# Performance work log

Measured on AMD Instinct MI355X. Metric: run time of the kernel, lower is better.

Reference implementation:

```python
import jax, jax.numpy as jnp
import numpy as np

D_MODEL = 1024
NUM_HEADS = 16
HEAD_DIM = D_MODEL // NUM_HEADS
THETA = 10000.0
MAX_SEQ_LEN = 2048
BATCH = 4
SEQ = 2048


def _rope_tables():
    # theta_vec = 1 / theta**(arange(0, d_k, 2)/d_k), pos outer product
    inv_freq = 1.0 / (THETA ** (jnp.arange(0, HEAD_DIM, 2, dtype=jnp.float32) / HEAD_DIM))
    pos = jnp.arange(MAX_SEQ_LEN, dtype=jnp.float32)
    freqs = jnp.outer(pos, inv_freq)  # [max_seq, head_dim//2]
    return jnp.cos(freqs), jnp.sin(freqs)


def apply_rope(x, cos, sin):
    # x: [..., S, d]; cos/sin: [S, d//2]; interleaved pairwise rotation
    x1 = x[..., 0::2]
    x2 = x[..., 1::2]
    o1 = x1 * cos - x2 * sin
    o2 = x2 * cos + x1 * sin
    return jnp.stack([o1, o2], axis=-1).reshape(x.shape)


def setup_inputs() -> dict:
    key = jax.random.key(0)
    kx, kq, kk, kv, ko = jax.random.split(key, 5)
    std = (1.0 / D_MODEL) ** 0.5
    x = jax.random.normal(kx, (BATCH, SEQ, D_MODEL), dtype=jnp.float32)
    w_q = jax.random.normal(kq, (D_MODEL, D_MODEL), dtype=jnp.float32) * std
    w_k = jax.random.normal(kk, (D_MODEL, D_MODEL), dtype=jnp.float32) * std
    w_v = jax.random.normal(kv, (D_MODEL, D_MODEL), dtype=jnp.float32) * std
    w_o = jax.random.normal(ko, (D_MODEL, D_MODEL), dtype=jnp.float32) * std
    cos, sin = _rope_tables()
    return {"x": x, "w_q": w_q, "w_k": w_k, "w_v": w_v, "w_o": w_o,
            "cos": cos, "sin": sin}


def reference(x, w_q, w_k, w_v, w_o, cos, sin):
    b, s, d = x.shape
    h, dk = NUM_HEADS, HEAD_DIM

    def proj(w):
        # einsum '... s d, hd d -> ... s hd' == x @ w.T, then split heads
        y = jnp.einsum('bsd,ed->bse', x, w)
        return y.reshape(b, s, h, dk).transpose(0, 2, 1, 3)  # [b,h,s,dk]

    q = apply_rope(proj(w_q), cos[:s], sin[:s])
    k = apply_rope(proj(w_k), cos[:s], sin[:s])
    v = proj(w_v)

    scores = jnp.einsum('bhnd,bhmd->bhnm', q, k) / (dk ** 0.5)
    causal = jnp.tril(jnp.ones((s, s), dtype=bool))
    scores = jnp.where(causal, scores, -jnp.inf)
    attn = jax.nn.softmax(scores, axis=-1)
    out = jnp.einsum('bhnm,bhmd->bhnd', attn, v)  # [b,h,s,dk]
    out = out.transpose(0, 2, 1, 3).reshape(b, s, d)
    # einsum '... s hd, d hd -> ... s d' == out @ w_o.T
    return jnp.einsum('bse,de->bsd', out, w_o)
```

## Files before the change

### kernel.cpp

```cpp
#include <hip/hip_runtime.h>
#include <hip/hip_bf16.h>


typedef __bf16 bf16;
typedef __bf16 bf16x8 __attribute__((ext_vector_type(8)));
typedef __bf16 bf16x4 __attribute__((ext_vector_type(4)));
typedef float f32x4 __attribute__((ext_vector_type(4)));

#define LOG2E 1.4426950408889634f
#define QSCALE (0.125f * LOG2E * 8388608.0f)
#define SEXP_SEED ((126.94269504f - 16.0f * LOG2E) * 8388608.0f)

__device__ __forceinline__ void async16(const void* g, void* l) {
  __builtin_amdgcn_global_load_lds(
      (const __attribute__((address_space(1))) void*)g,
      (__attribute__((address_space(3))) void*)l, 16, 0, 0);
}

#define MFMA16(a, b, c) __builtin_amdgcn_mfma_f32_16x16x32_bf16(a, b, c, 0, 0, 0)

__global__ void cast_all_kernel(const float* __restrict__ x,
                                const float* __restrict__ wq,
                                const float* __restrict__ wk,
                                const float* __restrict__ wv,
                                const float* __restrict__ wo,
                                const float* __restrict__ cosT,
                                const float* __restrict__ sinT,
                                bf16* __restrict__ xb, bf16* __restrict__ wb,
                                float2* __restrict__ csT) {
  int i = blockIdx.x * blockDim.x + threadIdx.x;
  if (i >= 3145728) {
    int j = i - 3145728;
    float2 cs;
    cs.x = cosT[j];
    cs.y = sinT[j];
    csT[j] = cs;
    return;
  }
  const float* src;
  bf16* dst;
  long o;
  if (i < 2097152) {
    src = x; dst = xb; o = i;
  } else {
    long j = i - 2097152;
    int w = (int)(j >> 18);
    o = j & 262143;
    src = (w == 0) ? wq : (w == 1) ? wk : (w == 2) ? wv : wo;
    dst = wb + (long)w * 1048576;
  }
  float4 v = reinterpret_cast<const float4*>(src)[o];
  bf16x4 out;
  out.x = (bf16)v.x; out.y = (bf16)v.y; out.z = (bf16)v.z; out.w = (bf16)v.w;
  *reinterpret_cast<bf16x4*>(dst + o * 4) = out;
}

template <int EPI, int TM, int TN>
__device__ __forceinline__ void gemm_dev(const bf16* __restrict__ A,
                                         const bf16* __restrict__ B,
                                         void* __restrict__ C, int N, int K,
                                         int bm, int bn, bf16* As, bf16* Bs,
                                         const float2* __restrict__ csT) {
  constexpr int WM = TM / 64;
  constexpr int WN = 4 / WM;
  constexpr int CW = TN / WN;
  constexpr int NT = CW / 16;
  constexpr int ROUNDS = (TM + TN) / 64;
  const int tid = threadIdx.x;
  const int wid = tid >> 6, lane = tid & 63;
  const int quad = lane >> 4, l15 = lane & 15;
  const int waveM = wid / WN, waveN = wid % WN;

  f32x4 acc[4][NT] = {};
  const bf16* Ag = A + (long)bm * TM * K;
  const bf16* Bg = B + (long)bn * TN * K;

  auto stage = [&](int buf, int k0) {
#pragma unroll
    for (int ri = 0; ri < ROUNDS; ++ri) {
      int c = ri * 256 + tid;
      int g = ri * 256 + (wid << 6);
      bool isA = g < TM * 4;
      int cl = isA ? c : c - TM * 4;
      int r = cl >> 2;
      int col = ((cl & 3) ^ ((r >> 1) & 3)) << 3;
      const bf16* src = (isA ? Ag : Bg) + (long)r * K + k0 + col;
      char* dst = isA ? ((char*)As + (long)buf * (TM * 64) + (long)g * 16)
                      : ((char*)Bs + (long)buf * (TN * 64) +
                         (long)(g - TM * 4) * 16);
      async16(src, dst);
    }
  };

  stage(0, 0);
  __syncthreads();
  int cur = 0;
  for (int k0 = 0; k0 < K; k0 += 32) {
    const bool more = (k0 + 32) < K;
    if (more) stage(cur ^ 1, k0 + 32);
    const bf16* Asb = As + cur * (TM * 32);
    const bf16* Bsb = Bs + cur * (TN * 32);
    bf16x8 af[4], bfr[NT];
#pragma unroll
    for (int t = 0; t < 4; ++t) {
      int rowA = waveM * 64 + t * 16 + l15;
      af[t] =
          *(const bf16x8*)(Asb + rowA * 32 + ((quad ^ ((rowA >> 1) & 3)) << 3));
    }
#pragma unroll
    for (int t = 0; t < NT; ++t) {
      int rowB = waveN * CW + t * 16 + l15;
      bfr[t] =
          *(const bf16x8*)(Bsb + rowB * 32 + ((quad ^ ((rowB >> 1) & 3)) << 3));
    }
#pragma unroll
    for (int mt = 0; mt < 4; ++mt)
#pragma unroll
      for (int nt = 0; nt < NT; ++nt)
        acc[mt][nt] = MFMA16(af[mt], bfr[nt], acc[mt][nt]);
    if (more) {
      __syncthreads();
      cur ^= 1;
    }
  }

  const float qsc = (EPI == 0 && bn < 8) ? QSCALE : 1.0f;
#pragma unroll
  for (int mt = 0; mt < 4; ++mt)
#pragma unroll
    for (int nt = 0; nt < NT; ++nt)
#pragma unroll
      for (int r = 0; r < 4; ++r) {
        int row = bm * TM + waveM * 64 + mt * 16 + quad * 4 + r;
        int col = bn * TN + waveN * CW + nt * 16 + l15;
        float v = acc[mt][nt][r];
        if (EPI == 0) {
          float pr = __shfl_xor(v, 1);
          int d = col & 63;
          float2 cs = csT[(row & 2047) * 32 + (d >> 1)];
          float o =
              (col & 1) ? (v * cs.x + pr * cs.y) : (v * cs.x - pr * cs.y);
          o *= qsc;
          long off = (long)(col >> 10) * 8388608 +
                     (long)(((row >> 11) << 4) + ((col >> 6) & 15)) * 131072 +
                     (long)(row & 2047) * 64 + d;
          ((bf16*)C)[off] = (bf16)o;
        } else if (EPI == 1) {
          long off = (long)(col >> 11) * 2097152 + (long)row * 2048 +
                     (col & 2047);
          ((bf16*)C)[off] = (bf16)v;
        } else {
          ((float*)C)[(long)row * N + col] = v;
        }
      }
}

__global__ __launch_bounds__(256) void gemm_qkv(const bf16* __restrict__ xb,
                                                const bf16* __restrict__ wqk,
                                                const bf16* __restrict__ wv,
                                                bf16* __restrict__ QK,
                                                bf16* __restrict__ VT,
                                                const float2* __restrict__ csT) {
  __shared__ __align__(16) bf16 As[2 * 128 * 32];
  __shared__ __align__(16) bf16 Bs[2 * 128 * 32];
  int p = blockIdx.x;
  if (p >= 1024) {
    int pv = p - 1024;
    int lv = (pv & 7) * 64 + (pv >> 3);
    gemm_dev<1, 128, 128>(wv, xb, VT, 8192, 1024, lv & 7, lv >> 3, As, Bs,
                          nullptr);
  } else {
    int l = (p & 7) * 128 + (p >> 3);
    gemm_dev<0, 128, 128>(xb, wqk, QK, 2048, 1024, l >> 4, l & 15, As, Bs,
                          csT);
  }
}

__global__ __launch_bounds__(256) void gemm_out(const bf16* __restrict__ A,
                                                const bf16* __restrict__ B,
                                                float* __restrict__ C) {
  __shared__ __align__(16) bf16 As[2 * 128 * 32];
  __shared__ __align__(16) bf16 Bs[2 * 128 * 32];
  int p = blockIdx.x;
  int l = (p & 7) * 64 + (p >> 3);
  gemm_dev<2, 128, 128>(A, B, C, 1024, 1024, l >> 3, l & 7, As, Bs, nullptr);
}

__device__ __forceinline__ void attn_step(const bf16* Ks, const bf16* Vs,
                                          bf16* Pw, const bf16x8* qf,
                                          const bf16x8 ones, f32x4* accO,
                                          f32x4& accL, int quad, int l15,
                                          int qloc, bool diag) {
  const int sw = l15 & 7;
  const f32x4 seedv = {SEXP_SEED, SEXP_SEED, SEXP_SEED, SEXP_SEED};
  f32x4 sacc[4] = {seedv, seedv, seedv, seedv};
#pragma unroll
  for (int mt = 0; mt < 4; ++mt)
#pragma unroll
    for (int kk = 0; kk < 2; ++kk) {
      bf16x8 kf = *(const bf16x8*)(Ks + (mt * 16 + l15) * 64 +
                                   ((((kk << 2) + quad) ^ sw) << 3));
      sacc[mt] = MFMA16(kf, qf[kk], sacc[mt]);
    }
  if (diag) {
#pragma unroll
    for (int mt = 0; mt < 4; ++mt)
#pragma unroll
      for (int r = 0; r < 4; ++r)
        if ((mt * 16 + quad * 4 + r) > qloc) sacc[mt][r] = 0.0f;
  }
#pragma unroll
  for (int mt = 0; mt < 4; ++mt) {
    int i0 = (int)sacc[mt][0], i1 = (int)sacc[mt][1];
    int i2 = (int)sacc[mt][2], i3 = (int)sacc[mt][3];
    uint2 pk;
    pk.x = __builtin_amdgcn_perm((unsigned)i1, (unsigned)i0, 0x07060302u);
    pk.y = __builtin_amdgcn_perm((unsigned)i3, (unsigned)i2, 0x07060302u);
    *(uint2*)(Pw + l15 * 88 + mt * 16 + quad * 4) = pk;
  }
  asm volatile("s_waitcnt lgkmcnt(0)" ::: "memory");
  bf16x8 pfr[2];
#pragma unroll
  for (int kk = 0; kk < 2; ++kk)
    pfr[kk] = *(const bf16x8*)(Pw + l15 * 88 + kk * 32 + quad * 8);
#pragma unroll
  for (int nt = 0; nt < 4; ++nt)
#pragma unroll
    for (int kk = 0; kk < 2; ++kk) {
      bf16x8 vf = *(const bf16x8*)(Vs + (nt * 16 + l15) * 64 +
                                   ((((kk << 2) + quad) ^ sw) << 3));
      accO[nt] = MFMA16(pfr[kk], vf, accO[nt]);
    }
#pragma unroll
  for (int kk = 0; kk < 2; ++kk)
    accL = MFMA16(pfr[kk], ones, accL);
}

__global__ __launch_bounds__(256, 4) void attn_kernel(
    const bf16* __restrict__ Q, const bf16* __restrict__ Kg,
    const bf16* __restrict__ VT, bf16* __restrict__ Out) {
  __shared__ __align__(16) bf16 Ks[64 * 64];
  __shared__ __align__(16) bf16 Vs[64 * 64];
  __shared__ __align__(16) bf16 Ps[4][16 * 88];
  const int tid = threadIdx.x, wid = tid >> 6, lane = tid & 63;
  const int quad = lane >> 4, l15 = lane & 15;
  const int id = blockIdx.x;
  const int p = (id >> 3) & 15;
  const int bh = (id & 7) * 8 + (id >> 7);
  const int q0t = p, q1t = 31 - p;
  const bf16* Qb = Q + (long)bh * 131072;
  const bf16* Kb = Kg + (long)bh * 131072;
  const bf16* Vb = VT + (long)bh * 131072;
  bf16* Pw = &Ps[wid][0];
  const int qloc = wid * 16 + l15;

  bf16x8 ones;
#pragma unroll
  for (int j = 0; j < 8; ++j) ones[j] = (bf16)1.0f;

  bf16x8 qf0[2], qf1[2];
#pragma unroll
  for (int kk = 0; kk < 2; ++kk) {
    qf0[kk] = *(const bf16x8*)(Qb + (long)(q0t * 64 + qloc) * 64 + kk * 32 +
                               quad * 8);
    qf1[kk] = *(const bf16x8*)(Qb + (long)(q1t * 64 + qloc) * 64 + kk * 32 +
                               quad * 8);
  }
  f32x4 acc0[4] = {}, acc1[4] = {};
  f32x4 accL0 = {}, accL1 = {};

  for (int kt = 0; kt <= q1t; ++kt) {
#pragma unroll
    for (int it = 0; it < 2; ++it) {
      int chunk = it * 256 + tid;
      int r = chunk >> 3;
      int c = (((chunk & 7) ^ (r & 7)) << 3);
      int ldsbase = (it * 256 + wid * 64) * 16;
      async16(Kb + (long)(kt * 64 + r) * 64 + c, (char*)Ks + ldsbase);
      async16(Vb + (long)r * 2048 + kt * 64 + c, (char*)Vs + ldsbase);
    }
    __syncthreads();
    attn_step(Ks, Vs, Pw, qf1, ones, acc1, accL1, quad, l15, qloc, kt == q1t);
    if (kt <= q0t)
      attn_step(Ks, Vs, Pw, qf0, ones, acc0, accL0, quad, l15, qloc,
                kt == q0t);
    __syncthreads();
  }

  const int b = bh >> 4, h = bh & 15;
#pragma unroll
  for (int r = 0; r < 4; ++r) {
    float lr0 = 1.0f / accL0[r];
    float lr1 = 1.0f / accL1[r];
#pragma unroll
    for (int nt = 0; nt < 4; ++nt) {
      int d = h * 64 + nt * 16 + l15;
      int qg0 = q0t * 64 + wid * 16 + quad * 4 + r;
      int qg1 = q1t * 64 + wid * 16 + quad * 4 + r;
      Out[(long)(b * 2048 + qg0) * 1024 + d] = (bf16)(acc0[nt][r] * lr0);
      Out[(long)(b * 2048 + qg1) * 1024 + d] = (bf16)(acc1[nt][r] * lr1);
    }
  }
}

extern "C" void kernel_launch(void* const* d_in, const int* in_sizes, int n_in,
                              void* d_out, int out_size, void* d_ws,
                              size_t ws_size, hipStream_t stream) {
  const float* x = (const float*)d_in[0];
  const float* w_q = (const float*)d_in[1];
  const float* w_k = (const float*)d_in[2];
  const float* w_v = (const float*)d_in[3];
  const float* w_o = (const float*)d_in[4];
  const float* cosT = (const float*)d_in[5];
  const float* sinT = (const float*)d_in[6];

  char* ws = (char*)d_ws;
  bf16* xb = (bf16*)(ws + 0);
  bf16* wqb = (bf16*)(ws + 16777216);
  bf16* wvb = (bf16*)(ws + 20971520);
  bf16* wob = (bf16*)(ws + 23068672);
  bf16* Qb = (bf16*)(ws + 25165824);
  bf16* Kb = (bf16*)(ws + 41943040);
  bf16* VTb = (bf16*)(ws + 58720256);
  float2* csT = (float2*)(ws + 75497472);
  bf16* attnb = xb;

  cast_all_kernel<<<12544, 256, 0, stream>>>(x, w_q, w_k, w_v, w_o, cosT,
                                             sinT, xb, wqb, csT);

  gemm_qkv<<<1536, 256, 0, stream>>>(xb, wqb, wvb, Qb, VTb, csT);

  attn_kernel<<<1024, 256, 0, stream>>>(Qb, Kb, VTb, attnb);

  gemm_out<<<512, 256, 0, stream>>>(attnb, wob, (float*)d_out);
}
```

Measured before the change: 244.5 us.

## Replace double-buffered K=32 GEMM staging with single-buffered K=64 tiles

The GEMM mainloop drops the double-buffered 32-wide K staging and instead loads 64-wide K tiles into one buffer, with a sync before compute and another before the next load. The LDS swizzle changes to an 8-chunk XOR pattern to suit the wider rows. This halves the number of K iterations and barriers, at the cost of no longer overlapping global loads with MFMA work, which can expose memory latency.

```diff
diff --git a/kernel.cpp b/kernel.cpp
--- a/kernel.cpp
+++ b/kernel.cpp
@@ -65,7 +65,7 @@
   constexpr int WN = 4 / WM;
   constexpr int CW = TN / WN;
   constexpr int NT = CW / 16;
-  constexpr int ROUNDS = (TM + TN) / 64;
+  constexpr int ROUNDS = (TM + TN) / 32;
   const int tid = threadIdx.x;
   const int wid = tid >> 6, lane = tid & 63;
   const int quad = lane >> 4, l15 = lane & 15;
@@ -75,53 +75,43 @@
   const bf16* Ag = A + (long)bm * TM * K;
   const bf16* Bg = B + (long)bn * TN * K;
 
-  auto stage = [&](int buf, int k0) {
+  for (int k0 = 0; k0 < K; k0 += 64) {
 #pragma unroll
     for (int ri = 0; ri < ROUNDS; ++ri) {
-      int c = ri * 256 + tid;
-      int g = ri * 256 + (wid << 6);
-      bool isA = g < TM * 4;
-      int cl = isA ? c : c - TM * 4;
-      int r = cl >> 2;
-      int col = ((cl & 3) ^ ((r >> 1) & 3)) << 3;
+      int ci = ri * 256 + tid;
+      int gb = ri * 256 + (wid << 6);
+      bool isA = gb < TM * 8;
+      int cl = isA ? ci : ci - TM * 8;
+      int r = cl >> 3;
+      int col = ((cl & 7) ^ (r & 7)) << 3;
       const bf16* src = (isA ? Ag : Bg) + (long)r * K + k0 + col;
-      char* dst = isA ? ((char*)As + (long)buf * (TM * 64) + (long)g * 16)
-                      : ((char*)Bs + (long)buf * (TN * 64) +
-                         (long)(g - TM * 4) * 16);
+      char* dst = isA ? ((char*)As + (long)ci * 16)
+                      : ((char*)Bs + (long)(ci - TM * 8) * 16);
       async16(src, dst);
     }
-  };
-
-  stage(0, 0);
-  __syncthreads();
-  int cur = 0;
-  for (int k0 = 0; k0 < K; k0 += 32) {
-    const bool more = (k0 + 32) < K;
-    if (more) stage(cur ^ 1, k0 + 32);
-    const bf16* Asb = As + cur * (TM * 32);
-    const bf16* Bsb = Bs + cur * (TN * 32);
-    bf16x8 af[4], bfr[NT];
-#pragma unroll
-    for (int t = 0; t < 4; ++t) {
-      int rowA = waveM * 64 + t * 16 + l15;
-      af[t] =
-          *(const bf16x8*)(Asb + rowA * 32 + ((quad ^ ((rowA >> 1) & 3)) << 3));
-    }
-#pragma unroll
-    for (int t = 0; t < NT; ++t) {
-      int rowB = waveN * CW + t * 16 + l15;
-      bfr[t] =
-          *(const bf16x8*)(Bsb + rowB * 32 + ((quad ^ ((rowB >> 1) & 3)) << 3));
-    }
-#pragma unroll
-    for (int mt = 0; mt < 4; ++mt)
-#pragma unroll
-      for (int nt = 0; nt < NT; ++nt)
-        acc[mt][nt] = MFMA16(af[mt], bfr[nt], acc[mt][nt]);
-    if (more) {
-      __syncthreads();
-      cur ^= 1;
-    }
+    __syncthreads();
+#pragma unroll
+    for (int kk = 0; kk < 2; ++kk) {
+      bf16x8 af[4], bfr[NT];
+#pragma unroll
+      for (int t = 0; t < 4; ++t) {
+        int rowA = waveM * 64 + t * 16 + l15;
+        af[t] = *(const bf16x8*)(As + rowA * 64 +
+                                 ((((kk << 2) + quad) ^ (rowA & 7)) << 3));
+      }
+#pragma unroll
+      for (int t = 0; t < NT; ++t) {
+        int rowB = waveN * CW + t * 16 + l15;
+        bfr[t] = *(const bf16x8*)(Bs + rowB * 64 +
+                                  ((((kk << 2) + quad) ^ (rowB & 7)) << 3));
+      }
+#pragma unroll
+      for (int mt = 0; mt < 4; ++mt)
+#pragma unroll
+        for (int nt = 0; nt < NT; ++nt)
+          acc[mt][nt] = MFMA16(af[mt], bfr[nt], acc[mt][nt]);
+    }
+    if (k0 + 64 < K) __syncthreads();
   }
 
   const float qsc = (EPI == 0 && bn < 8) ? QSCALE : 1.0f;
@@ -161,8 +151,8 @@
                                                 bf16* __restrict__ QK,
                                                 bf16* __restrict__ VT,
                                                 const float2* __restrict__ csT) {
-  __shared__ __align__(16) bf16 As[2 * 128 * 32];
-  __shared__ __align__(16) bf16 Bs[2 * 128 * 32];
+  __shared__ __align__(16) bf16 As[128 * 64];
+  __shared__ __align__(16) bf16 Bs[128 * 64];
   int p = blockIdx.x;
   if (p >= 1024) {
     int pv = p - 1024;
@@ -179,8 +169,8 @@
 __global__ __launch_bounds__(256) void gemm_out(const bf16* __restrict__ A,
                                                 const bf16* __restrict__ B,
                                                 float* __restrict__ C) {
-  __shared__ __align__(16) bf16 As[2 * 128 * 32];
-  __shared__ __align__(16) bf16 Bs[2 * 128 * 32];
+  __shared__ __align__(16) bf16 As[128 * 64];
+  __shared__ __align__(16) bf16 Bs[128 * 64];
   int p = blockIdx.x;
   int l = (p & 7) * 64 + (p >> 3);
   gemm_dev<2, 128, 128>(A, B, C, 1024, 1024, l >> 3, l & 7, As, Bs, nullptr);
```

Result: faster. 235.7 us, median of 2 (-3.6%).
